# Kernel optimization log

Hardware: AMD Instinct MI355X
Metric: run time of the kernel (lower is better)

Reference implementation:

```python
import jax, jax.numpy as jnp
import numpy as np

N_NODES = 98304
N_GRAPHS = 2048
NODES_PER_GRAPH = 48
N_EDGES = 393216
NODE_IN = 128
EMB = 64
HID = 256
N_LAYERS = 6
ATTN_DIM = 256
N_HEADS = 4
HEAD_DIM = ATTN_DIM // N_HEADS
OUT_DIM = 1024


def setup_inputs() -> dict:
    key = jax.random.key(0)
    ks = iter(jax.random.split(key, 40))

    def nrm(shape, fan_in):
        return (jax.random.normal(next(ks), shape, dtype=jnp.float32)
                / np.float32(np.sqrt(fan_in)))

    x = jax.random.normal(next(ks), (N_NODES, NODE_IN), dtype=jnp.float32)
    edge_index = jax.random.randint(next(ks), (2, N_EDGES), 0, N_NODES, dtype=jnp.int32)
    batch = (jnp.arange(N_NODES, dtype=jnp.int32) // NODES_PER_GRAPH)

    inp = {
        "x": x,
        "edge_index": edge_index,
        "batch": batch,
        "W_embed": nrm((NODE_IN, EMB), NODE_IN),
        "b_embed": jnp.zeros((EMB,), jnp.float32),
        "W1": nrm((N_LAYERS, EMB, HID), EMB),
        "b1": jnp.zeros((N_LAYERS, HID), jnp.float32),
        "W2": nrm((N_LAYERS, HID, 2 * HID), HID),
        "b2": jnp.zeros((N_LAYERS, 2 * HID), jnp.float32),
        "W3": nrm((N_LAYERS, 2 * HID, EMB), 2 * HID),
        "b3": jnp.zeros((N_LAYERS, EMB), jnp.float32),
        "Wp": nrm((EMB, ATTN_DIM), EMB),
        "bp": jnp.zeros((ATTN_DIM,), jnp.float32),
        "q": jax.random.normal(next(ks), (1, ATTN_DIM), dtype=jnp.float32),
        "W_in": nrm((ATTN_DIM, 3 * ATTN_DIM), ATTN_DIM),
        "b_in": jnp.zeros((3 * ATTN_DIM,), jnp.float32),
        "W_out": nrm((ATTN_DIM, ATTN_DIM), ATTN_DIM),
        "b_out": jnp.zeros((ATTN_DIM,), jnp.float32),
        "Wh1": nrm((ATTN_DIM, HID), ATTN_DIM),
        "bh1": jnp.zeros((HID,), jnp.float32),
        "ln_g": jnp.ones((HID,), jnp.float32),
        "ln_b": jnp.zeros((HID,), jnp.float32),
        "Wh2": nrm((HID, OUT_DIM), HID),
        "bh2": jnp.zeros((OUT_DIM,), jnp.float32),
    }
    return inp


def _forward(x, edge_index, batch, W_embed, b_embed, W1, b1, W2, b2, W3, b3,
             Wp, bp, q, W_in, b_in, W_out, b_out, Wh1, bh1, ln_g, ln_b, Wh2, bh2):
    row = edge_index[0]  # only row is used, matching the torch module

    # node embed
    h = x @ W_embed + b_embed  # [N, 64]

    # 6 GNN layers: gather h[row] -> 3-layer MLP -> scatter_add back to row
    for l in range(N_LAYERS):
        m = jax.nn.relu(h[row] @ W1[l] + b1[l])          # [E, 256]
        m = jax.nn.relu(m @ W2[l] + b2[l])               # [E, 512]
        dh = m @ W3[l] + b3[l]                           # [E, 64]
        h = h + jax.ops.segment_sum(dh, row, num_segments=N_NODES)

    # attention pooling per graph (single learned query, 4 heads)
    hp = h @ Wp + bp                                     # [N, 256]
    Wq, Wk, Wv = W_in[:, :ATTN_DIM], W_in[:, ATTN_DIM:2 * ATTN_DIM], W_in[:, 2 * ATTN_DIM:]
    bq, bk, bv = b_in[:ATTN_DIM], b_in[ATTN_DIM:2 * ATTN_DIM], b_in[2 * ATTN_DIM:]

    qh = ((q @ Wq + bq).reshape(N_HEADS, HEAD_DIM)
          / jnp.asarray(np.sqrt(HEAD_DIM), jnp.float32))  # [H, D]
    k = (hp @ Wk + bk).reshape(N_NODES, N_HEADS, HEAD_DIM)
    v = (hp @ Wv + bv).reshape(N_NODES, N_HEADS, HEAD_DIM)

    scores = jnp.einsum('nhd,hd->nh', k, qh)             # [N, H]
    smax = jax.ops.segment_max(scores, batch, num_segments=N_GRAPHS)  # [B, H]
    e = jnp.exp(scores - smax[batch])
    denom = jax.ops.segment_sum(e, batch, num_segments=N_GRAPHS)      # [B, H]
    w = e / denom[batch]                                  # [N, H]
    pooled = jax.ops.segment_sum(w[:, :, None] * v, batch, num_segments=N_GRAPHS)  # [B, H, D]
    attn = pooled.reshape(N_GRAPHS, ATTN_DIM) @ W_out + b_out  # [B, 256]

    # projection head: ReLU -> Linear -> ReLU -> LayerNorm -> Linear
    t = jax.nn.relu(attn) @ Wh1 + bh1
    t = jax.nn.relu(t)
    mu = jnp.mean(t, axis=-1, keepdims=True)
    var = jnp.mean((t - mu) ** 2, axis=-1, keepdims=True)
    t = (t - mu) * jax.lax.rsqrt(var + 1e-5) * ln_g + ln_b
    return t @ Wh2 + bh2                                  # [B, 1024]


def reference(x, edge_index, batch, W_embed, b_embed, W1, b1, W2, b2, W3, b3,
              Wp, bp, q, W_in, b_in, W_out, b_out, Wh1, bh1, ln_g, ln_b, Wh2, bh2):
    return _forward(x, edge_index, batch, W_embed, b_embed, W1, b1, W2, b2, W3, b3,
                    Wp, bp, q, W_in, b_in, W_out, b_out, Wh1, bh1, ln_g, ln_b, Wh2, bh2)
```

## Files before the change

kernel.cpp:

```cpp
#include <hip/hip_runtime.h>
#include <hip/hip_bf16.h>

#define N_NODES 98304
#define N_GRAPHS 2048
#define N_EDGES 393216
#define EMB 64
#define HID 256
#define N_LAYERS_ 6

typedef __attribute__((ext_vector_type(8))) short short8v;
typedef __attribute__((ext_vector_type(4))) float f32x4;
#define MFMA16(a, b, c) __builtin_amdgcn_mfma_f32_16x16x32_bf16(a, b, c, 0, 0, 0)

__device__ __forceinline__ unsigned short f2bf(float x) {
    unsigned int u = __float_as_uint(x);
    u = (u + 0x7fffu + ((u >> 16) & 1u)) >> 16;
    return (unsigned short)u;
}
__device__ __forceinline__ float bf2f(unsigned short h) {
    return __uint_as_float(((unsigned int)h) << 16);
}
__device__ __forceinline__ unsigned int cvtpk(float a, float b) {
    unsigned int r;
    asm("v_cvt_pk_bf16_f32 %0, %1, %2" : "=v"(r) : "v"(a), "v"(b));
    return r;
}
__device__ __forceinline__ int swz(int row, int col, int rowc) {
    return (row * rowc + col) ^ ((row & ((rowc >> 3) - 1)) << 3);
}

__global__ __launch_bounds__(256) void zero_cnt_kernel(int* __restrict__ cnt) {
    int i = blockIdx.x * 256 + threadIdx.x;
    if (i < N_NODES) cnt[i] = 0;
}
__global__ __launch_bounds__(256) void hist_kernel(const int* __restrict__ row,
                                                   int* __restrict__ cnt) {
    int i = blockIdx.x * 256 + threadIdx.x;
    if (i < N_EDGES) atomicAdd(&cnt[row[i]], 1);
}

__global__ __launch_bounds__(64) void prep_frag_kernel(
    const float* __restrict__ W, unsigned short* __restrict__ oh,
    unsigned short* __restrict__ ol, int K, int N)
{
    const int NF = N >> 4, KS = K >> 5;
    const int fpl = NF * KS;
    const int layer = blockIdx.x / fpl;
    const int fid = blockIdx.x % fpl;
    const int nf = fid / KS, ks = fid % KS;
    const int lane = threadIdx.x;
    const float* Wl = W + (size_t)layer * K * N;
    const int n = nf * 16 + (lane & 15);
    const int kb = ks * 32 + (lane >> 4) * 8;
    short8v vh, vl;
    #pragma unroll
    for (int j = 0; j < 8; j++) {
        float wv = Wl[(size_t)(kb + j) * N + n];
        unsigned short hi = f2bf(wv);
        vh[j] = (short)hi;
        vl[j] = (short)f2bf(wv - bf2f(hi));
    }
    size_t o = (size_t)layer * K * N + ((size_t)(nf * KS + ks) * 64 + lane) * 8;
    *reinterpret_cast<short8v*>(oh + o) = vh;
    *reinterpret_cast<short8v*>(ol + o) = vl;
}

__global__ __launch_bounds__(256) void gbuild_kernel(
    const float* __restrict__ Wp, const float* __restrict__ bp,
    const float* __restrict__ W_in, const float* __restrict__ b_in,
    float* __restrict__ Gm, float* __restrict__ Gd)
{
    const int idx = blockIdx.x * 256 + threadIdx.x;
    const int q = idx >> 8, p = idx & 255;
    float s = 0.f;
    if ((q >> 6) == (p >> 6)) {
        const float* wr = Wp + (q & 63) * 256;
        for (int j = 0; j < 256; j++) s += wr[j] * W_in[j * 768 + 512 + p];
    }
    Gm[q * 256 + p] = s;
    if (blockIdx.x == 0) {
        const int pp = threadIdx.x;
        float dsum = b_in[512 + pp];
        for (int j = 0; j < 256; j++) dsum += bp[j] * W_in[j * 768 + 512 + pp];
        Gd[pp] = dsum;
    }
}

__global__ __launch_bounds__(256) void embed_mfma_kernel(
    const float* __restrict__ x,
    const unsigned short* __restrict__ Weh, const unsigned short* __restrict__ Wel,
    const float* __restrict__ b, float* __restrict__ h)
{
    __shared__ __attribute__((aligned(16))) unsigned short xh[32 * 128];
    __shared__ __attribute__((aligned(16))) unsigned short xl[32 * 128];
    const int tid = threadIdx.x;
    const int lane = tid & 63, w = tid >> 6;
    const int lm = lane & 15, lq = lane >> 4;
    const int base = blockIdx.x * 32;
    {
        int row = tid >> 3, c0 = (tid & 7) * 16;
        const float4* p = reinterpret_cast<const float4*>(x + (size_t)(base + row) * 128 + c0);
        #pragma unroll
        for (int g = 0; g < 4; g++) {
            float4 u = p[g];
            unsigned int p01 = cvtpk(u.x, u.y);
            unsigned int p23 = cvtpk(u.z, u.w);
            float h0 = __uint_as_float(p01 << 16), h1 = __uint_as_float(p01 & 0xffff0000u);
            float h2 = __uint_as_float(p23 << 16), h3 = __uint_as_float(p23 & 0xffff0000u);
            unsigned int q01 = cvtpk(u.x - h0, u.y - h1);
            unsigned int q23 = cvtpk(u.z - h2, u.w - h3);
            int idx = swz(row, c0 + g * 4, 128);
            *reinterpret_cast<uint2*>(&xh[idx]) = make_uint2(p01, p23);
            *reinterpret_cast<uint2*>(&xl[idx]) = make_uint2(q01, q23);
        }
    }
    __syncthreads();
    f32x4 acc0, acc1;
    {
        float bv = b[w * 16 + lm];
        acc0 = f32x4{bv, bv, bv, bv};
        acc1 = acc0;
    }
    #pragma unroll
    for (int ks = 0; ks < 4; ks++) {
        short8v a0h = *reinterpret_cast<const short8v*>(&xh[swz(lm, ks * 32 + lq * 8, 128)]);
        short8v a0l = *reinterpret_cast<const short8v*>(&xl[swz(lm, ks * 32 + lq * 8, 128)]);
        short8v a1h = *reinterpret_cast<const short8v*>(&xh[swz(16 + lm, ks * 32 + lq * 8, 128)]);
        short8v a1l = *reinterpret_cast<const short8v*>(&xl[swz(16 + lm, ks * 32 + lq * 8, 128)]);
        size_t bi = ((size_t)(w * 4 + ks) * 64 + lane) * 8;
        short8v bh = *reinterpret_cast<const short8v*>(Weh + bi);
        short8v bl = *reinterpret_cast<const short8v*>(Wel + bi);
        acc0 = MFMA16(a0h, bh, acc0); acc0 = MFMA16(a0l, bh, acc0); acc0 = MFMA16(a0h, bl, acc0);
        acc1 = MFMA16(a1h, bh, acc1); acc1 = MFMA16(a1l, bh, acc1); acc1 = MFMA16(a1h, bl, acc1);
    }
    #pragma unroll
    for (int r = 0; r < 4; r++) {
        h[(size_t)(base + lq * 4 + r) * 64 + w * 16 + lm] = acc0[r];
        h[(size_t)(base + 16 + lq * 4 + r) * 64 + w * 16 + lm] = acc1[r];
    }
}

__device__ __forceinline__ void store_quad(
    unsigned short* __restrict__ oh, unsigned short* __restrict__ ol,
    float v0, float v1, float v2, float v3,
    int row0, int col, int rowc)
{
    unsigned int p01 = cvtpk(v0, v1);
    unsigned int p23 = cvtpk(v2, v3);
    float h0 = __uint_as_float(p01 << 16), h1 = __uint_as_float(p01 & 0xffff0000u);
    float h2 = __uint_as_float(p23 << 16), h3 = __uint_as_float(p23 & 0xffff0000u);
    unsigned int q01 = cvtpk(v0 - h0, v1 - h1);
    unsigned int q23 = cvtpk(v2 - h2, v3 - h3);
    oh[swz(row0 + 0, col, rowc)] = (unsigned short)p01;
    oh[swz(row0 + 1, col, rowc)] = (unsigned short)(p01 >> 16);
    oh[swz(row0 + 2, col, rowc)] = (unsigned short)p23;
    oh[swz(row0 + 3, col, rowc)] = (unsigned short)(p23 >> 16);
    ol[swz(row0 + 0, col, rowc)] = (unsigned short)q01;
    ol[swz(row0 + 1, col, rowc)] = (unsigned short)(q01 >> 16);
    ol[swz(row0 + 2, col, rowc)] = (unsigned short)q23;
    ol[swz(row0 + 3, col, rowc)] = (unsigned short)(q23 >> 16);
}

__global__ __launch_bounds__(512, 4) void layer_mfma_kernel(
    float* __restrict__ h, const int* __restrict__ cnt,
    const unsigned short* __restrict__ W1h, const unsigned short* __restrict__ W1l,
    const float* __restrict__ b1,
    const unsigned short* __restrict__ W2h, const unsigned short* __restrict__ W2l,
    const float* __restrict__ b2,
    const unsigned short* __restrict__ W3h, const unsigned short* __restrict__ W3l,
    const float* __restrict__ b3)
{
    __shared__ __attribute__((aligned(16))) unsigned short m1h_[8192];
    __shared__ __attribute__((aligned(16))) unsigned short m1l_[8192];
    __shared__ __attribute__((aligned(16))) unsigned short m2b_[16384];
    unsigned short* hsh = m2b_;
    unsigned short* hsl = m2b_ + 2048;
    const int tid = threadIdx.x;
    const int lane = tid & 63, w = tid >> 6;
    const int lm = lane & 15, lq = lane >> 4;
    const int base = blockIdx.x * 32;

    int s0row = tid >> 4, s0c = (tid & 15) * 4;
    const float4 u0 = *reinterpret_cast<const float4*>(h + (size_t)(base + s0row) * 64 + s0c);

    const unsigned short* pAh = W1h + ((size_t)(4 * w) * 64 + lane) * 8;
    const unsigned short* pAl = W1l + ((size_t)(4 * w) * 64 + lane) * 8;
    short8v awh[4], awl[4];
    #pragma unroll
    for (int i = 0; i < 4; i++) {
        awh[i] = *reinterpret_cast<const short8v*>(pAh + (size_t)i * 512);
        awl[i] = *reinterpret_cast<const short8v*>(pAl + (size_t)i * 512);
    }

    {
        unsigned int p01 = cvtpk(u0.x, u0.y);
        unsigned int p23 = cvtpk(u0.z, u0.w);
        float h0 = __uint_as_float(p01 << 16), h1 = __uint_as_float(p01 & 0xffff0000u);
        float h2 = __uint_as_float(p23 << 16), h3 = __uint_as_float(p23 & 0xffff0000u);
        unsigned int q01 = cvtpk(u0.x - h0, u0.y - h1);
        unsigned int q23 = cvtpk(u0.z - h2, u0.w - h3);
        int idx = swz(s0row, s0c, 64);
        *reinterpret_cast<uint2*>(&hsh[idx]) = make_uint2(p01, p23);
        *reinterpret_cast<uint2*>(&hsl[idx]) = make_uint2(q01, q23);
    }
    __syncthreads();

    {
        f32x4 acc[2][2];
        #pragma unroll
        for (int f = 0; f < 2; f++) {
            float bv = b1[(2 * w + f) * 16 + lm];
            acc[f][0] = f32x4{bv, bv, bv, bv};
            acc[f][1] = acc[f][0];
        }
        __builtin_amdgcn_s_setprio(1);
        #pragma unroll
        for (int ks = 0; ks < 2; ks++) {
            short8v ah0 = *reinterpret_cast<const short8v*>(&hsh[swz(lm, ks * 32 + lq * 8, 64)]);
            short8v al0 = *reinterpret_cast<const short8v*>(&hsl[swz(lm, ks * 32 + lq * 8, 64)]);
            short8v ah1 = *reinterpret_cast<const short8v*>(&hsh[swz(16 + lm, ks * 32 + lq * 8, 64)]);
            short8v al1 = *reinterpret_cast<const short8v*>(&hsl[swz(16 + lm, ks * 32 + lq * 8, 64)]);
            #pragma unroll
            for (int f = 0; f < 2; f++) {
                short8v bh = awh[2 * f + ks];
                short8v bl = awl[2 * f + ks];
                acc[f][0] = MFMA16(ah0, bh, acc[f][0]);
                acc[f][0] = MFMA16(al0, bh, acc[f][0]);
                acc[f][0] = MFMA16(ah0, bl, acc[f][0]);
                acc[f][1] = MFMA16(ah1, bh, acc[f][1]);
                acc[f][1] = MFMA16(al1, bh, acc[f][1]);
                acc[f][1] = MFMA16(ah1, bl, acc[f][1]);
            }
        }
        __builtin_amdgcn_s_setprio(0);
        #pragma unroll
        for (int f = 0; f < 2; f++)
            #pragma unroll
            for (int m = 0; m < 2; m++)
                store_quad(m1h_, m1l_,
                           fmaxf(acc[f][m][0], 0.f), fmaxf(acc[f][m][1], 0.f),
                           fmaxf(acc[f][m][2], 0.f), fmaxf(acc[f][m][3], 0.f),
                           m * 16 + lq * 4, (2 * w + f) * 16 + lm, 256);
    }
    __syncthreads();

    const int nfc = w & 3, kq = w >> 2;
    f32x4 dacc[2];
    if (kq == 0) {
        float bv = b3[nfc * 16 + lm];
        dacc[0] = f32x4{bv, bv, bv, bv};
    } else {
        dacc[0] = f32x4{0.f, 0.f, 0.f, 0.f};
    }
    dacc[1] = dacc[0];

    #pragma unroll
    for (int c = 0; c < 4; ++c) {
        unsigned short* m2h_ = m2b_ + (c & 1) * 8192;
        unsigned short* m2l_ = m2h_ + 4096;
        short8v cwh[2], cwl[2];
        {
            const int nfg = c * 8 + w;
            const unsigned short* pBh = W2h + ((size_t)(nfg * 8) * 64 + lane) * 8;
            const unsigned short* pBl = W2l + ((size_t)(nfg * 8) * 64 + lane) * 8;
            f32x4 acc[2];
            {
                float bv = b2[nfg * 16 + lm];
                acc[0] = f32x4{bv, bv, bv, bv};
                acc[1] = acc[0];
            }
            short8v whE = *reinterpret_cast<const short8v*>(pBh);
            short8v wlE = *reinterpret_cast<const short8v*>(pBl);
            short8v whO = *reinterpret_cast<const short8v*>(pBh + 512);
            short8v wlO = *reinterpret_cast<const short8v*>(pBl + 512);
            __builtin_amdgcn_s_setprio(1);
            #pragma unroll
            for (int kp = 0; kp < 4; kp++) {
                const int k0 = 2 * kp;
                short8v whE2, wlE2, whO2, wlO2;
                if (kp < 3) {
                    whE2 = *reinterpret_cast<const short8v*>(pBh + (size_t)(k0 + 2) * 512);
                    wlE2 = *reinterpret_cast<const short8v*>(pBl + (size_t)(k0 + 2) * 512);
                    whO2 = *reinterpret_cast<const short8v*>(pBh + (size_t)(k0 + 3) * 512);
                    wlO2 = *reinterpret_cast<const short8v*>(pBl + (size_t)(k0 + 3) * 512);
                }
                {
                    short8v ah0 = *reinterpret_cast<const short8v*>(&m1h_[swz(lm, k0 * 32 + lq * 8, 256)]);
                    short8v al0 = *reinterpret_cast<const short8v*>(&m1l_[swz(lm, k0 * 32 + lq * 8, 256)]);
                    short8v ah1 = *reinterpret_cast<const short8v*>(&m1h_[swz(16 + lm, k0 * 32 + lq * 8, 256)]);
                    short8v al1 = *reinterpret_cast<const short8v*>(&m1l_[swz(16 + lm, k0 * 32 + lq * 8, 256)]);
                    acc[0] = MFMA16(ah0, whE, acc[0]);
                    acc[0] = MFMA16(al0, whE, acc[0]);
                    acc[0] = MFMA16(ah0, wlE, acc[0]);
                    acc[1] = MFMA16(ah1, whE, acc[1]);
                    acc[1] = MFMA16(al1, whE, acc[1]);
                    acc[1] = MFMA16(ah1, wlE, acc[1]);
                }
                {
                    short8v ah0 = *reinterpret_cast<const short8v*>(&m1h_[swz(lm, (k0 + 1) * 32 + lq * 8, 256)]);
                    short8v al0 = *reinterpret_cast<const short8v*>(&m1l_[swz(lm, (k0 + 1) * 32 + lq * 8, 256)]);
                    short8v ah1 = *reinterpret_cast<const short8v*>(&m1h_[swz(16 + lm, (k0 + 1) * 32 + lq * 8, 256)]);
                    short8v al1 = *reinterpret_cast<const short8v*>(&m1l_[swz(16 + lm, (k0 + 1) * 32 + lq * 8, 256)]);
                    acc[0] = MFMA16(ah0, whO, acc[0]);
                    acc[0] = MFMA16(al0, whO, acc[0]);
                    acc[0] = MFMA16(ah0, wlO, acc[0]);
                    acc[1] = MFMA16(ah1, whO, acc[1]);
                    acc[1] = MFMA16(al1, whO, acc[1]);
                    acc[1] = MFMA16(ah1, wlO, acc[1]);
                }
                if (kp < 3) { whE = whE2; wlE = wlE2; whO = whO2; wlO = wlO2; }
            }
            __builtin_amdgcn_s_setprio(0);
            #pragma unroll
            for (int kl = 0; kl < 2; kl++) {
                size_t bi = ((size_t)(nfc * 16 + c * 4 + kq * 2 + kl) * 64 + lane) * 8;
                cwh[kl] = *reinterpret_cast<const short8v*>(W3h + bi);
                cwl[kl] = *reinterpret_cast<const short8v*>(W3l + bi);
            }
            #pragma unroll
            for (int m = 0; m < 2; m++)
                store_quad(m2h_, m2l_,
                           fmaxf(acc[m][0], 0.f), fmaxf(acc[m][1], 0.f),
                           fmaxf(acc[m][2], 0.f), fmaxf(acc[m][3], 0.f),
                           m * 16 + lq * 4, w * 16 + lm, 128);
        }
        __syncthreads();
        {
            __builtin_amdgcn_s_setprio(1);
            #pragma unroll
            for (int kl = 0; kl < 2; kl++) {
                int ksl = kq * 2 + kl;
                short8v ah0 = *reinterpret_cast<const short8v*>(&m2h_[swz(lm, ksl * 32 + lq * 8, 128)]);
                short8v al0 = *reinterpret_cast<const short8v*>(&m2l_[swz(lm, ksl * 32 + lq * 8, 128)]);
                short8v ah1 = *reinterpret_cast<const short8v*>(&m2h_[swz(16 + lm, ksl * 32 + lq * 8, 128)]);
                short8v al1 = *reinterpret_cast<const short8v*>(&m2l_[swz(16 + lm, ksl * 32 + lq * 8, 128)]);
                dacc[0] = MFMA16(ah0, cwh[kl], dacc[0]);
                dacc[0] = MFMA16(al0, cwh[kl], dacc[0]);
                dacc[0] = MFMA16(ah0, cwl[kl], dacc[0]);
                dacc[1] = MFMA16(ah1, cwh[kl], dacc[1]);
                dacc[1] = MFMA16(al1, cwh[kl], dacc[1]);
                dacc[1] = MFMA16(ah1, cwl[kl], dacc[1]);
            }
            __builtin_amdgcn_s_setprio(0);
        }
    }

    float* scr = reinterpret_cast<float*>(m1h_);
    if (kq == 1) {
        #pragma unroll
        for (int m = 0; m < 2; m++)
            #pragma unroll
            for (int r = 0; r < 4; r++)
                scr[(m * 16 + lq * 4 + r) * 64 + nfc * 16 + lm] = dacc[m][r];
    }
    __syncthreads();
    if (kq == 0) {
        #pragma unroll
        for (int m = 0; m < 2; m++)
            #pragma unroll
            for (int r = 0; r < 4; r++) {
                int rr = base + m * 16 + lq * 4 + r;
                float dv = dacc[m][r] + scr[(m * 16 + lq * 4 + r) * 64 + nfc * 16 + lm];
                size_t gi = (size_t)rr * 64 + nfc * 16 + lm;
                h[gi] = h[gi] + (float)cnt[rr] * dv;
            }
    }
}

__global__ __launch_bounds__(256) void prec_kernel(
    const float* __restrict__ q, const float* __restrict__ W_in,
    const float* __restrict__ b_in, const float* __restrict__ Wp,
    const float* __restrict__ bp, float* __restrict__ prec)
{
    __shared__ float qh_s[256];
    __shared__ float u_s[4 * 256];
    const int tid = threadIdx.x;
    {
        float acc = b_in[tid];
        for (int j = 0; j < 256; j++) acc += q[j] * W_in[j * 768 + tid];
        qh_s[tid] = acc * 0.125f;
    }
    __syncthreads();
    {
        #pragma unroll
        for (int hd = 0; hd < 4; hd++) {
            float a = 0.f;
            for (int d = 0; d < 64; d++)
                a += W_in[tid * 768 + 256 + hd * 64 + d] * qh_s[hd * 64 + d];
            u_s[hd * 256 + tid] = a;
        }
    }
    __syncthreads();
    {
        int hd = tid >> 6, i = tid & 63;
        float a = 0.f;
        for (int j = 0; j < 256; j++) a += Wp[i * 256 + j] * u_s[hd * 256 + j];
        prec[hd * 64 + i] = a;
    }
    if (tid < 4) {
        float a = 0.f;
        for (int j = 0; j < 256; j++) a += bp[j] * u_s[tid * 256 + j];
        for (int d = 0; d < 64; d++) a += b_in[256 + tid * 64 + d] * qh_s[tid * 64 + d];
        prec[256 + tid] = a;
    }
}

__global__ __launch_bounds__(64) void attnpool_kernel(
    const float* __restrict__ h, const float* __restrict__ prec,
    float* __restrict__ hw)
{
    __shared__ float hs[48 * 65];
    __shared__ float ss[4 * 64];
    __shared__ float ds_[4];
    __shared__ float wl[48 * 4];
    const int lane = threadIdx.x;
    const int g = blockIdx.x;
    #pragma unroll
    for (int hd = 0; hd < 4; hd++) ss[hd * 64 + lane] = prec[hd * 64 + lane];
    if (lane < 4) ds_[lane] = prec[256 + lane];
    for (int r = 0; r < 48; r++)
        hs[r * 65 + lane] = h[((size_t)g * 48 + r) * 64 + lane];
    __syncthreads();
    float sc[4] = {0.f, 0.f, 0.f, 0.f};
    if (lane < 48) {
        #pragma unroll
        for (int hd = 0; hd < 4; hd++) sc[hd] = ds_[hd];
        for (int c = 0; c < 64; c++) {
            float a = hs[lane * 65 + c];
            #pragma unroll
            for (int hd = 0; hd < 4; hd++) sc[hd] += a * ss[hd * 64 + c];
        }
    }
    #pragma unroll
    for (int hd = 0; hd < 4; hd++) {
        float v = (lane < 48) ? sc[hd] : -3.0e38f;
        #pragma unroll
        for (int m = 32; m >= 1; m >>= 1) v = fmaxf(v, __shfl_xor(v, m, 64));
        float e = (lane < 48) ? __expf(sc[hd] - v) : 0.f;
        float s = e;
        #pragma unroll
        for (int m = 32; m >= 1; m >>= 1) s += __shfl_xor(s, m, 64);
        if (lane < 48) wl[lane * 4 + hd] = e / s;
    }
    __syncthreads();
    float acc[4] = {0.f, 0.f, 0.f, 0.f};
    for (int n = 0; n < 48; n++) {
        float hv = hs[n * 65 + lane];
        #pragma unroll
        for (int hd = 0; hd < 4; hd++) acc[hd] += wl[n * 4 + hd] * hv;
    }
    #pragma unroll
    for (int hd = 0; hd < 4; hd++) hw[(size_t)g * 256 + hd * 64 + lane] = acc[hd];
}

__device__ __forceinline__ void tail_stage(
    const unsigned short* __restrict__ inh, const unsigned short* __restrict__ inl,
    const unsigned short* __restrict__ wh, const unsigned short* __restrict__ wl,
    const float* __restrict__ bias, const bool do_relu,
    unsigned short* __restrict__ oth, unsigned short* __restrict__ otl,
    float* __restrict__ tf32,
    const int w, const int lane, const int lm, const int lq)
{
    f32x4 acc[2][2];
    #pragma unroll
    for (int f = 0; f < 2; f++) {
        float bv = bias[(2 * w + f) * 16 + lm];
        acc[f][0] = f32x4{bv, bv, bv, bv};
        acc[f][1] = acc[f][0];
    }
    #pragma unroll
    for (int ks = 0; ks < 8; ks++) {
        short8v ah0 = *reinterpret_cast<const short8v*>(&inh[swz(lm, ks * 32 + lq * 8, 256)]);
        short8v al0 = *reinterpret_cast<const short8v*>(&inl[swz(lm, ks * 32 + lq * 8, 256)]);
        short8v ah1 = *reinterpret_cast<const short8v*>(&inh[swz(16 + lm, ks * 32 + lq * 8, 256)]);
        short8v al1 = *reinterpret_cast<const short8v*>(&inl[swz(16 + lm, ks * 32 + lq * 8, 256)]);
        #pragma unroll
        for (int f = 0; f < 2; f++) {
            size_t bi = ((size_t)((2 * w + f) * 8 + ks) * 64 + lane) * 8;
            short8v bh = *reinterpret_cast<const short8v*>(wh + bi);
            short8v bl = *reinterpret_cast<const short8v*>(wl + bi);
            acc[f][0] = MFMA16(ah0, bh, acc[f][0]);
            acc[f][0] = MFMA16(al0, bh, acc[f][0]);
            acc[f][0] = MFMA16(ah0, bl, acc[f][0]);
            acc[f][1] = MFMA16(ah1, bh, acc[f][1]);
            acc[f][1] = MFMA16(al1, bh, acc[f][1]);
            acc[f][1] = MFMA16(ah1, bl, acc[f][1]);
        }
    }
    #pragma unroll
    for (int f = 0; f < 2; f++)
        #pragma unroll
        for (int m = 0; m < 2; m++) {
            if (tf32) {
                #pragma unroll
                for (int r = 0; r < 4; r++) {
                    float v = acc[f][m][r];
                    if (do_relu) v = fmaxf(v, 0.f);
                    tf32[(m * 16 + lq * 4 + r) * 256 + (2 * w + f) * 16 + lm] = v;
                }
            } else {
                float v0 = acc[f][m][0], v1 = acc[f][m][1], v2 = acc[f][m][2], v3 = acc[f][m][3];
                if (do_relu) {
                    v0 = fmaxf(v0, 0.f); v1 = fmaxf(v1, 0.f);
                    v2 = fmaxf(v2, 0.f); v3 = fmaxf(v3, 0.f);
                }
                store_quad(oth, otl, v0, v1, v2, v3,
                           m * 16 + lq * 4, (2 * w + f) * 16 + lm, 256);
            }
        }
}

__global__ __launch_bounds__(512, 4) void tail_mfma_kernel(
    const float* __restrict__ hw,
    const unsigned short* __restrict__ Gh, const unsigned short* __restrict__ Gl,
    const float* __restrict__ Gd,
    const unsigned short* __restrict__ Woh, const unsigned short* __restrict__ Wol,
    const float* __restrict__ b_out,
    const unsigned short* __restrict__ Wh1h, const unsigned short* __restrict__ Wh1l,
    const float* __restrict__ bh1,
    const float* __restrict__ ln_g, const float* __restrict__ ln_b,
    const unsigned short* __restrict__ Wh2h, const unsigned short* __restrict__ Wh2l,
    const float* __restrict__ bh2,
    float* __restrict__ out)
{
    __shared__ __attribute__((aligned(16))) unsigned short L[32768];
    unsigned short* Ah = L;
    unsigned short* Al = L + 8192;
    unsigned short* Bh = L + 16384;
    unsigned short* Bl = L + 24576;
    float* tf = reinterpret_cast<float*>(L + 16384);
    const int tid = threadIdx.x;
    const int lane = tid & 63, w = tid >> 6;
    const int lm = lane & 15, lq = lane >> 4;
    const int g0 = blockIdx.x * 32;

    {
        const float4* hp = reinterpret_cast<const float4*>(hw + (size_t)g0 * 256);
        #pragma unroll
        for (int i = 0; i < 4; i++) {
            int e = tid + 512 * i;
            int row = e >> 6, c0 = (e & 63) * 4;
            float4 u = hp[e];
            unsigned int p01 = cvtpk(u.x, u.y);
            unsigned int p23 = cvtpk(u.z, u.w);
            float h0 = __uint_as_float(p01 << 16), h1 = __uint_as_float(p01 & 0xffff0000u);
            float h2 = __uint_as_float(p23 << 16), h3 = __uint_as_float(p23 & 0xffff0000u);
            unsigned int q01 = cvtpk(u.x - h0, u.y - h1);
            unsigned int q23 = cvtpk(u.z - h2, u.w - h3);
            int idx = swz(row, c0, 256);
            *reinterpret_cast<uint2*>(&Ah[idx]) = make_uint2(p01, p23);
            *reinterpret_cast<uint2*>(&Al[idx]) = make_uint2(q01, q23);
        }
    }
    __syncthreads();
    tail_stage(Ah, Al, Gh, Gl, Gd, false, Bh, Bl, nullptr, w, lane, lm, lq);
    __syncthreads();
    tail_stage(Bh, Bl, Woh, Wol, b_out, true, Ah, Al, nullptr, w, lane, lm, lq);
    __syncthreads();
    tail_stage(Ah, Al, Wh1h, Wh1l, bh1, true, nullptr, nullptr, tf, w, lane, lm, lq);
    __syncthreads();
    {
        const int row = tid >> 4, l16 = tid & 15;
        float s = 0.f;
        #pragma unroll
        for (int k = 0; k < 16; k++) s += tf[row * 256 + l16 + 16 * k];
        #pragma unroll
        for (int m = 1; m < 16; m <<= 1) s += __shfl_xor(s, m, 16);
        float mu = s * (1.f / 256.f);
        float v = 0.f;
        #pragma unroll
        for (int k = 0; k < 16; k++) {
            float d = tf[row * 256 + l16 + 16 * k] - mu;
            v += d * d;
        }
        #pragma unroll
        for (int m = 1; m < 16; m <<= 1) v += __shfl_xor(v, m, 16);
        float rs = rsqrtf(v * (1.f / 256.f) + 1e-5f);
        #pragma unroll
        for (int k = 0; k < 16; k++) {
            int col = l16 + 16 * k;
            float val = (tf[row * 256 + col] - mu) * rs * ln_g[col] + ln_b[col];
            unsigned short hi = f2bf(val);
            int idx = swz(row, col, 256);
            Ah[idx] = hi;
            Al[idx] = f2bf(val - bf2f(hi));
        }
    }
    __syncthreads();
    {
        f32x4 acc[8][2];
        #pragma unroll
        for (int f = 0; f < 8; f++) {
            float bv = bh2[(8 * w + f) * 16 + lm];
            acc[f][0] = f32x4{bv, bv, bv, bv};
            acc[f][1] = acc[f][0];
        }
        #pragma unroll
        for (int ks = 0; ks < 8; ks++) {
            short8v ah0 = *reinterpret_cast<const short8v*>(&Ah[swz(lm, ks * 32 + lq * 8, 256)]);
            short8v al0 = *reinterpret_cast<const short8v*>(&Al[swz(lm, ks * 32 + lq * 8, 256)]);
            short8v ah1 = *reinterpret_cast<const short8v*>(&Ah[swz(16 + lm, ks * 32 + lq * 8, 256)]);
            short8v al1 = *reinterpret_cast<const short8v*>(&Al[swz(16 + lm, ks * 32 + lq * 8, 256)]);
            #pragma unroll
            for (int f = 0; f < 8; f++) {
                size_t bi = ((size_t)((8 * w + f) * 8 + ks) * 64 + lane) * 8;
                short8v bh = *reinterpret_cast<const short8v*>(Wh2h + bi);
                short8v bl = *reinterpret_cast<const short8v*>(Wh2l + bi);
                acc[f][0] = MFMA16(ah0, bh, acc[f][0]);
                acc[f][0] = MFMA16(al0, bh, acc[f][0]);
                acc[f][0] = MFMA16(ah0, bl, acc[f][0]);
                acc[f][1] = MFMA16(ah1, bh, acc[f][1]);
                acc[f][1] = MFMA16(al1, bh, acc[f][1]);
                acc[f][1] = MFMA16(ah1, bl, acc[f][1]);
            }
        }
        #pragma unroll
        for (int f = 0; f < 8; f++)
            #pragma unroll
            for (int m = 0; m < 2; m++)
                #pragma unroll
                for (int r = 0; r < 4; r++)
                    out[(size_t)(g0 + m * 16 + lq * 4 + r) * 1024 + (8 * w + f) * 16 + lm]
                        = acc[f][m][r];
    }
}

extern "C" void kernel_launch(void* const* d_in, const int* in_sizes, int n_in,
                              void* d_out, int out_size, void* d_ws, size_t ws_size,
                              hipStream_t stream) {
    const float* x       = (const float*)d_in[0];
    const int*   edge    = (const int*)d_in[1];
    const float* W_embed = (const float*)d_in[3];
    const float* b_embed = (const float*)d_in[4];
    const float* W1 = (const float*)d_in[5];
    const float* b1 = (const float*)d_in[6];
    const float* W2 = (const float*)d_in[7];
    const float* b2 = (const float*)d_in[8];
    const float* W3 = (const float*)d_in[9];
    const float* b3 = (const float*)d_in[10];
    const float* Wp = (const float*)d_in[11];
    const float* bp = (const float*)d_in[12];
    const float* q  = (const float*)d_in[13];
    const float* W_in  = (const float*)d_in[14];
    const float* b_in  = (const float*)d_in[15];
    const float* W_out = (const float*)d_in[16];
    const float* b_out = (const float*)d_in[17];
    const float* Wh1 = (const float*)d_in[18];
    const float* bh1 = (const float*)d_in[19];
    const float* ln_g = (const float*)d_in[20];
    const float* ln_b = (const float*)d_in[21];
    const float* Wh2 = (const float*)d_in[22];
    const float* bh2 = (const float*)d_in[23];
    float* out = (float*)d_out;

    char* ws = (char*)d_ws;
    int*   cnt  = (int*)(ws + 0);
    float* h    = (float*)(ws + 393216);
    float* hw   = (float*)(ws + 25559040);
    float* prec = (float*)(ws + 27656192);
    unsigned short* W1h = (unsigned short*)(ws + 27657232);
    unsigned short* W1l = (unsigned short*)(ws + 27853840);
    unsigned short* W2h = (unsigned short*)(ws + 28050448);
    unsigned short* W2l = (unsigned short*)(ws + 29623312);
    unsigned short* W3h = (unsigned short*)(ws + 31196176);
    unsigned short* W3l = (unsigned short*)(ws + 31589392);
    unsigned short* Weh = (unsigned short*)(ws + 31982608);
    unsigned short* Wel = (unsigned short*)(ws + 31998992);
    float* Gm  = (float*)(ws + 32015376);
    float* Gd  = (float*)(ws + 32277520);
    unsigned short* Gfh  = (unsigned short*)(ws + 32278544);
    unsigned short* Gfl  = (unsigned short*)(ws + 32409616);
    unsigned short* Wofh = (unsigned short*)(ws + 32540688);
    unsigned short* Wofl = (unsigned short*)(ws + 32671760);
    unsigned short* Wh1fh= (unsigned short*)(ws + 32802832);
    unsigned short* Wh1fl= (unsigned short*)(ws + 32933904);
    unsigned short* Wh2fh= (unsigned short*)(ws + 33064976);
    unsigned short* Wh2fl= (unsigned short*)(ws + 33589264);

    zero_cnt_kernel<<<N_NODES / 256, 256, 0, stream>>>(cnt);
    hist_kernel<<<N_EDGES / 256, 256, 0, stream>>>(edge, cnt);

    prep_frag_kernel<<<1 * (64 / 16) * (128 / 32), 64, 0, stream>>>(W_embed, Weh, Wel, 128, 64);
    prep_frag_kernel<<<6 * (256 / 16) * (64 / 32), 64, 0, stream>>>(W1, W1h, W1l, 64, 256);
    prep_frag_kernel<<<6 * (512 / 16) * (256 / 32), 64, 0, stream>>>(W2, W2h, W2l, 256, 512);
    prep_frag_kernel<<<6 * (64 / 16) * (512 / 32), 64, 0, stream>>>(W3, W3h, W3l, 512, 64);

    gbuild_kernel<<<256, 256, 0, stream>>>(Wp, bp, W_in, b_in, Gm, Gd);
    prep_frag_kernel<<<(256 / 16) * (256 / 32), 64, 0, stream>>>(Gm, Gfh, Gfl, 256, 256);
    prep_frag_kernel<<<(256 / 16) * (256 / 32), 64, 0, stream>>>(W_out, Wofh, Wofl, 256, 256);
    prep_frag_kernel<<<(256 / 16) * (256 / 32), 64, 0, stream>>>(Wh1, Wh1fh, Wh1fl, 256, 256);
    prep_frag_kernel<<<(1024 / 16) * (256 / 32), 64, 0, stream>>>(Wh2, Wh2fh, Wh2fl, 256, 1024);

    embed_mfma_kernel<<<N_NODES / 32, 256, 0, stream>>>(x, Weh, Wel, b_embed, h);
    for (int l = 0; l < N_LAYERS_; l++) {
        layer_mfma_kernel<<<N_NODES / 32, 512, 0, stream>>>(
            h, cnt,
            W1h + (size_t)l * EMB * HID,     W1l + (size_t)l * EMB * HID,     b1 + (size_t)l * HID,
            W2h + (size_t)l * HID * 2 * HID, W2l + (size_t)l * HID * 2 * HID, b2 + (size_t)l * 2 * HID,
            W3h + (size_t)l * 2 * HID * EMB, W3l + (size_t)l * 2 * HID * EMB, b3 + (size_t)l * EMB);
    }
    prec_kernel<<<1, 256, 0, stream>>>(q, W_in, b_in, Wp, bp, prec);
    attnpool_kernel<<<N_GRAPHS, 64, 0, stream>>>(h, prec, hw);
    tail_mfma_kernel<<<N_GRAPHS / 32, 512, 0, stream>>>(
        hw, Gfh, Gfl, Gd, Wofh, Wofl, b_out, Wh1fh, Wh1fl, bh1,
        ln_g, ln_b, Wh2fh, Wh2fl, bh2, out);
}
```

Before: 851.3 us.

## Restructure W2/W3 chain into two 256-wide halves with fewer barriers

Replaces the four 128-column chunks of the second GEMM, each followed by a barrier and a partial third GEMM, with two 256-column halves. Each wave now computes two feature tiles per half, so every A fragment read from LDS feeds more MFMAs and only one m2 buffer is used. The change cuts the number of barriers and LDS re-reads of m1. In exchange it drops the explicit register prefetch of W2 fragments and the double-buffered m2, which removes some overlap between phases and raises register pressure from the doubled accumulators.

```diff
diff --git a/kernel.cpp b/kernel.cpp
--- a/kernel.cpp
+++ b/kernel.cpp
@@ -172,9 +172,13 @@
 {
     __shared__ __attribute__((aligned(16))) unsigned short m1h_[8192];
     __shared__ __attribute__((aligned(16))) unsigned short m1l_[8192];
-    __shared__ __attribute__((aligned(16))) unsigned short m2b_[16384];
-    unsigned short* hsh = m2b_;
-    unsigned short* hsl = m2b_ + 2048;
+    __shared__ __attribute__((aligned(16))) unsigned short m2_[16384];
+    unsigned short* m2h_ = m2_;
+    unsigned short* m2l_ = m2_ + 8192;
+    unsigned short* hsh = m2_;
+    unsigned short* hsl = m2_ + 2048;
+    float* scr = reinterpret_cast<float*>(m1h_);
+
     const int tid = threadIdx.x;
     const int lane = tid & 63, w = tid >> 6;
     const int lm = lane & 15, lq = lane >> 4;
@@ -254,98 +258,135 @@
     }
     dacc[1] = dacc[0];
 
-    #pragma unroll
-    for (int c = 0; c < 4; ++c) {
-        unsigned short* m2h_ = m2b_ + (c & 1) * 8192;
-        unsigned short* m2l_ = m2h_ + 4096;
-        short8v cwh[2], cwl[2];
-        {
-            const int nfg = c * 8 + w;
-            const unsigned short* pBh = W2h + ((size_t)(nfg * 8) * 64 + lane) * 8;
-            const unsigned short* pBl = W2l + ((size_t)(nfg * 8) * 64 + lane) * 8;
-            f32x4 acc[2];
-            {
-                float bv = b2[nfg * 16 + lm];
-                acc[0] = f32x4{bv, bv, bv, bv};
-                acc[1] = acc[0];
+    f32x4 accB[2][2];
+
+    {
+        const int nfg0 = 2 * w;
+        #pragma unroll
+        for (int f = 0; f < 2; f++) {
+            float bv = b2[(nfg0 + f) * 16 + lm];
+            accB[f][0] = f32x4{bv, bv, bv, bv};
+            accB[f][1] = accB[f][0];
+        }
+        __builtin_amdgcn_s_setprio(1);
+        #pragma unroll
+        for (int ks = 0; ks < 8; ks++) {
+            short8v ah0 = *reinterpret_cast<const short8v*>(&m1h_[swz(lm, ks * 32 + lq * 8, 256)]);
+            short8v al0 = *reinterpret_cast<const short8v*>(&m1l_[swz(lm, ks * 32 + lq * 8, 256)]);
+            short8v ah1 = *reinterpret_cast<const short8v*>(&m1h_[swz(16 + lm, ks * 32 + lq * 8, 256)]);
+            short8v al1 = *reinterpret_cast<const short8v*>(&m1l_[swz(16 + lm, ks * 32 + lq * 8, 256)]);
+            #pragma unroll
+            for (int f = 0; f < 2; f++) {
+                size_t bi = ((size_t)((nfg0 + f) * 8 + ks) * 64 + lane) * 8;
+                short8v bh = *reinterpret_cast<const short8v*>(W2h + bi);
+                short8v bl = *reinterpret_cast<const short8v*>(W2l + bi);
+                accB[f][0] = MFMA16(ah0, bh, accB[f][0]);
+                accB[f][0] = MFMA16(al0, bh, accB[f][0]);
+                accB[f][0] = MFMA16(ah0, bl, accB[f][0]);
+                accB[f][1] = MFMA16(ah1, bh, accB[f][1]);
+                accB[f][1] = MFMA16(al1, bh, accB[f][1]);
+                accB[f][1] = MFMA16(ah1, bl, accB[f][1]);
             }
-            short8v whE = *reinterpret_cast<const short8v*>(pBh);
-            short8v wlE = *reinterpret_cast<const short8v*>(pBl);
-            short8v whO = *reinterpret_cast<const short8v*>(pBh + 512);
-            short8v wlO = *reinterpret_cast<const short8v*>(pBl + 512);
-            __builtin_amdgcn_s_setprio(1);
-            #pragma unroll
-            for (int kp = 0; kp < 4; kp++) {
-                const int k0 = 2 * kp;
-                short8v whE2, wlE2, whO2, wlO2;
-                if (kp < 3) {
-                    whE2 = *reinterpret_cast<const short8v*>(pBh + (size_t)(k0 + 2) * 512);
-                    wlE2 = *reinterpret_cast<const short8v*>(pBl + (size_t)(k0 + 2) * 512);
-                    whO2 = *reinterpret_cast<const short8v*>(pBh + (size_t)(k0 + 3) * 512);
-                    wlO2 = *reinterpret_cast<const short8v*>(pBl + (size_t)(k0 + 3) * 512);
-                }
-                {
-                    short8v ah0 = *reinterpret_cast<const short8v*>(&m1h_[swz(lm, k0 * 32 + lq * 8, 256)]);
-                    short8v al0 = *reinterpret_cast<const short8v*>(&m1l_[swz(lm, k0 * 32 + lq * 8, 256)]);
-                    short8v ah1 = *reinterpret_cast<const short8v*>(&m1h_[swz(16 + lm, k0 * 32 + lq * 8, 256)]);
-                    short8v al1 = *reinterpret_cast<const short8v*>(&m1l_[swz(16 + lm, k0 * 32 + lq * 8, 256)]);
-                    acc[0] = MFMA16(ah0, whE, acc[0]);
-                    acc[0] = MFMA16(al0, whE, acc[0]);
-                    acc[0] = MFMA16(ah0, wlE, acc[0]);
-                    acc[1] = MFMA16(ah1, whE, acc[1]);
-                    acc[1] = MFMA16(al1, whE, acc[1]);
-                    acc[1] = MFMA16(ah1, wlE, acc[1]);
-                }
-                {
-                    short8v ah0 = *reinterpret_cast<const short8v*>(&m1h_[swz(lm, (k0 + 1) * 32 + lq * 8, 256)]);
-                    short8v al0 = *reinterpret_cast<const short8v*>(&m1l_[swz(lm, (k0 + 1) * 32 + lq * 8, 256)]);
-                    short8v ah1 = *reinterpret_cast<const short8v*>(&m1h_[swz(16 + lm, (k0 + 1) * 32 + lq * 8, 256)]);
-                    short8v al1 = *reinterpret_cast<const short8v*>(&m1l_[swz(16 + lm, (k0 + 1) * 32 + lq * 8, 256)]);
-                    acc[0] = MFMA16(ah0, whO, acc[0]);
-                    acc[0] = MFMA16(al0, whO, acc[0]);
-                    acc[0] = MFMA16(ah0, wlO, acc[0]);
-                    acc[1] = MFMA16(ah1, whO, acc[1]);
-                    acc[1] = MFMA16(al1, whO, acc[1]);
-                    acc[1] = MFMA16(ah1, wlO, acc[1]);
-                }
-                if (kp < 3) { whE = whE2; wlE = wlE2; whO = whO2; wlO = wlO2; }
-            }
-            __builtin_amdgcn_s_setprio(0);
-            #pragma unroll
-            for (int kl = 0; kl < 2; kl++) {
-                size_t bi = ((size_t)(nfc * 16 + c * 4 + kq * 2 + kl) * 64 + lane) * 8;
-                cwh[kl] = *reinterpret_cast<const short8v*>(W3h + bi);
-                cwl[kl] = *reinterpret_cast<const short8v*>(W3l + bi);
-            }
+        }
+        __builtin_amdgcn_s_setprio(0);
+        #pragma unroll
+        for (int f = 0; f < 2; f++)
             #pragma unroll
             for (int m = 0; m < 2; m++)
                 store_quad(m2h_, m2l_,
-                           fmaxf(acc[m][0], 0.f), fmaxf(acc[m][1], 0.f),
-                           fmaxf(acc[m][2], 0.f), fmaxf(acc[m][3], 0.f),
-                           m * 16 + lq * 4, w * 16 + lm, 128);
-        }
-        __syncthreads();
-        {
-            __builtin_amdgcn_s_setprio(1);
-            #pragma unroll
-            for (int kl = 0; kl < 2; kl++) {
-                int ksl = kq * 2 + kl;
-                short8v ah0 = *reinterpret_cast<const short8v*>(&m2h_[swz(lm, ksl * 32 + lq * 8, 128)]);
-                short8v al0 = *reinterpret_cast<const short8v*>(&m2l_[swz(lm, ksl * 32 + lq * 8, 128)]);
-                short8v ah1 = *reinterpret_cast<const short8v*>(&m2h_[swz(16 + lm, ksl * 32 + lq * 8, 128)]);
-                short8v al1 = *reinterpret_cast<const short8v*>(&m2l_[swz(16 + lm, ksl * 32 + lq * 8, 128)]);
-                dacc[0] = MFMA16(ah0, cwh[kl], dacc[0]);
-                dacc[0] = MFMA16(al0, cwh[kl], dacc[0]);
-                dacc[0] = MFMA16(ah0, cwl[kl], dacc[0]);
-                dacc[1] = MFMA16(ah1, cwh[kl], dacc[1]);
-                dacc[1] = MFMA16(al1, cwh[kl], dacc[1]);
-                dacc[1] = MFMA16(ah1, cwl[kl], dacc[1]);
+                           fmaxf(accB[f][m][0], 0.f), fmaxf(accB[f][m][1], 0.f),
+                           fmaxf(accB[f][m][2], 0.f), fmaxf(accB[f][m][3], 0.f),
+                           m * 16 + lq * 4, (2 * w + f) * 16 + lm, 256);
+    }
+    __syncthreads();
+
+    {
+        __builtin_amdgcn_s_setprio(1);
+        #pragma unroll
+        for (int kl = 0; kl < 4; kl++) {
+            int ksl = kq * 4 + kl;
+            short8v ah0 = *reinterpret_cast<const short8v*>(&m2h_[swz(lm, ksl * 32 + lq * 8, 256)]);
+            short8v al0 = *reinterpret_cast<const short8v*>(&m2l_[swz(lm, ksl * 32 + lq * 8, 256)]);
+            short8v ah1 = *reinterpret_cast<const short8v*>(&m2h_[swz(16 + lm, ksl * 32 + lq * 8, 256)]);
+            short8v al1 = *reinterpret_cast<const short8v*>(&m2l_[swz(16 + lm, ksl * 32 + lq * 8, 256)]);
+            size_t bi = ((size_t)(nfc * 16 + ksl) * 64 + lane) * 8;
+            short8v ch = *reinterpret_cast<const short8v*>(W3h + bi);
+            short8v cl = *reinterpret_cast<const short8v*>(W3l + bi);
+            dacc[0] = MFMA16(ah0, ch, dacc[0]);
+            dacc[0] = MFMA16(al0, ch, dacc[0]);
+            dacc[0] = MFMA16(ah0, cl, dacc[0]);
+            dacc[1] = MFMA16(ah1, ch, dacc[1]);
+            dacc[1] = MFMA16(al1, ch, dacc[1]);
+            dacc[1] = MFMA16(ah1, cl, dacc[1]);
+        }
+        __builtin_amdgcn_s_setprio(0);
+    }
+    {
+        const int nfg0 = 16 + 2 * w;
+        #pragma unroll
+        for (int f = 0; f < 2; f++) {
+            float bv = b2[(nfg0 + f) * 16 + lm];
+            accB[f][0] = f32x4{bv, bv, bv, bv};
+            accB[f][1] = accB[f][0];
+        }
+        __builtin_amdgcn_s_setprio(1);
+        #pragma unroll
+        for (int ks = 0; ks < 8; ks++) {
+            short8v ah0 = *reinterpret_cast<const short8v*>(&m1h_[swz(lm, ks * 32 + lq * 8, 256)]);
+            short8v al0 = *reinterpret_cast<const short8v*>(&m1l_[swz(lm, ks * 32 + lq * 8, 256)]);
+            short8v ah1 = *reinterpret_cast<const short8v*>(&m1h_[swz(16 + lm, ks * 32 + lq * 8, 256)]);
+            short8v al1 = *reinterpret_cast<const short8v*>(&m1l_[swz(16 + lm, ks * 32 + lq * 8, 256)]);
+            #pragma unroll
+            for (int f = 0; f < 2; f++) {
+                size_t bi = ((size_t)((nfg0 + f) * 8 + ks) * 64 + lane) * 8;
+                short8v bh = *reinterpret_cast<const short8v*>(W2h + bi);
+                short8v bl = *reinterpret_cast<const short8v*>(W2l + bi);
+                accB[f][0] = MFMA16(ah0, bh, accB[f][0]);
+                accB[f][0] = MFMA16(al0, bh, accB[f][0]);
+                accB[f][0] = MFMA16(ah0, bl, accB[f][0]);
+                accB[f][1] = MFMA16(ah1, bh, accB[f][1]);
+                accB[f][1] = MFMA16(al1, bh, accB[f][1]);
+                accB[f][1] = MFMA16(ah1, bl, accB[f][1]);
             }
-            __builtin_amdgcn_s_setprio(0);
-        }
-    }
-
-    float* scr = reinterpret_cast<float*>(m1h_);
+        }
+        __builtin_amdgcn_s_setprio(0);
+    }
+    __syncthreads();
+
+    {
+        #pragma unroll
+        for (int f = 0; f < 2; f++)
+            #pragma unroll
+            for (int m = 0; m < 2; m++)
+                store_quad(m2h_, m2l_,
+                           fmaxf(accB[f][m][0], 0.f), fmaxf(accB[f][m][1], 0.f),
+                           fmaxf(accB[f][m][2], 0.f), fmaxf(accB[f][m][3], 0.f),
+                           m * 16 + lq * 4, (2 * w + f) * 16 + lm, 256);
+    }
+    __syncthreads();
+
+    {
+        __builtin_amdgcn_s_setprio(1);
+        #pragma unroll
+        for (int kl = 0; kl < 4; kl++) {
+            int ksl = kq * 4 + kl;
+            short8v ah0 = *reinterpret_cast<const short8v*>(&m2h_[swz(lm, ksl * 32 + lq * 8, 256)]);
+            short8v al0 = *reinterpret_cast<const short8v*>(&m2l_[swz(lm, ksl * 32 + lq * 8, 256)]);
+            short8v ah1 = *reinterpret_cast<const short8v*>(&m2h_[swz(16 + lm, ksl * 32 + lq * 8, 256)]);
+            short8v al1 = *reinterpret_cast<const short8v*>(&m2l_[swz(16 + lm, ksl * 32 + lq * 8, 256)]);
+            size_t bi = ((size_t)(nfc * 16 + 8 + ksl) * 64 + lane) * 8;
+            short8v ch = *reinterpret_cast<const short8v*>(W3h + bi);
+            short8v cl = *reinterpret_cast<const short8v*>(W3l + bi);
+            dacc[0] = MFMA16(ah0, ch, dacc[0]);
+            dacc[0] = MFMA16(al0, ch, dacc[0]);
+            dacc[0] = MFMA16(ah0, cl, dacc[0]);
+            dacc[1] = MFMA16(ah1, ch, dacc[1]);
+            dacc[1] = MFMA16(al1, ch, dacc[1]);
+            dacc[1] = MFMA16(ah1, cl, dacc[1]);
+        }
+        __builtin_amdgcn_s_setprio(0);
+    }
+
     if (kq == 1) {
         #pragma unroll
         for (int m = 0; m < 2; m++)
```

Measured after the change: 865.4 us. About the same (+1.7%).
